# Optimization experiments

Measured on AMD Instinct MI355X. Metric: run time of the kernel, lower is better.

## Reference

```python
import jax, jax.numpy as jnp
import numpy as np

B, N, CIN, COUT, NS, S = 16, 512, 512, 512, 16, 8
EPS = 1e-5


def _bn(y, g, b):
    # eval-mode BatchNorm1d: running_mean=0, running_var=1 (fresh module buffers)
    return y * (g / jnp.sqrt(1.0 + EPS)) + b


def setup_inputs():
    key = jax.random.key(0)
    ks = jax.random.split(key, 16)

    def lin(k, fi, fo):
        kw, kb = jax.random.split(k)
        s = 1.0 / np.sqrt(fi)
        return (jax.random.uniform(kw, (fi, fo), minval=-s, maxval=s),
                jax.random.uniform(kb, (fo,), minval=-s, maxval=s))

    Wq, bq = lin(ks[0], CIN, COUT)
    Wk, bk = lin(ks[1], CIN, COUT)
    Wv, bv = lin(ks[2], CIN, COUT)
    p1_W, p1_b = lin(ks[3], 3, 3)
    p2_W, p2_b = lin(ks[4], 3, COUT)
    w1_W, w1_b = lin(ks[5], COUT, COUT // S)
    w2_W, w2_b = lin(ks[6], COUT // S, COUT // S)
    return dict(
        p=jax.random.uniform(ks[7], (B, N, 3)),
        x=jax.random.normal(ks[8], (B, CIN, N)),
        Wq=Wq, bq=bq, Wk=Wk, bk=bk, Wv=Wv, bv=bv,
        p1_W=p1_W, p1_b=p1_b,
        p_bn_g=1.0 + 0.1 * jax.random.normal(ks[9], (3,)),
        p_bn_b=0.1 * jax.random.normal(ks[10], (3,)),
        p2_W=p2_W, p2_b=p2_b,
        w_bn1_g=1.0 + 0.1 * jax.random.normal(ks[11], (COUT,)),
        w_bn1_b=0.1 * jax.random.normal(ks[12], (COUT,)),
        w1_W=w1_W, w1_b=w1_b,
        w_bn2_g=1.0 + 0.1 * jax.random.normal(ks[13], (COUT // S,)),
        w_bn2_b=0.1 * jax.random.normal(ks[14], (COUT // S,)),
        w2_W=w2_W, w2_b=w2_b,
    )


def reference(p, x, Wq, bq, Wk, bk, Wv, bv, p1_W, p1_b, p_bn_g, p_bn_b,
              p2_W, p2_b, w_bn1_g, w_bn1_b, w1_W, w1_b, w_bn2_g, w_bn2_b,
              w2_W, w2_b):
    xt = x.transpose(0, 2, 1)                     # (B,N,CIN)
    xq = xt @ Wq + bq                             # (B,N,COUT)
    xk = xt @ Wk + bk
    xv = xt @ Wv + bv
    # kNN over points (self-query): squared distances, then 16 smallest
    sq = jnp.sum(p * p, axis=-1)                  # (B,N)
    d = sq[:, :, None] + sq[:, None, :] - 2.0 * jnp.einsum('bnd,bmd->bnm', p, p)
    _, idx = jax.lax.top_k(-d, NS)                # (B,N,NS), includes self
    gather = jax.vmap(lambda f, i: f[i])          # per-batch fancy gather
    k_g = gather(xk, idx)                         # (B,N,NS,COUT)
    v_g = gather(xv, idx)                         # (B,N,NS,COUT)
    p_r = gather(p, idx) - p[:, :, None, :]       # relative coords (B,N,NS,3)
    # linear_p: Linear(3,3) -> BN(3) -> ReLU -> Linear(3,COUT)
    pr = jax.nn.relu(_bn(p_r @ p1_W + p1_b, p_bn_g, p_bn_b)) @ p2_W + p2_b
    # vector attention logits; out_planes//mid_planes == 1 so the .sum(3) is identity
    w = k_g - xq[:, :, None, :] + pr              # (B,N,NS,COUT)
    # linear_w: BN -> ReLU -> Linear(C, C//s) -> BN -> ReLU -> Linear(C//s, C//s)
    w = jax.nn.relu(_bn(w, w_bn1_g, w_bn1_b)) @ w1_W + w1_b
    w = jax.nn.relu(_bn(w, w_bn2_g, w_bn2_b)) @ w2_W + w2_b
    w = jax.nn.softmax(w, axis=2)                 # softmax over neighbors
    out = ((v_g + pr).reshape(B, N, NS, S, COUT // S)
           * w[:, :, :, None, :]).sum(2)          # (B,N,S,COUT//S)
    return out.reshape(B, N, COUT)
```

## Files before the change

kernel.cpp:

```cpp
#include <hip/hip_runtime.h>

typedef unsigned short u16;
typedef unsigned int   u32;

#define Bv  16
#define Nv  512
#define Cv  512
#define NSv 16
#define CCv 64

typedef __attribute__((ext_vector_type(8))) short bf16x8;
typedef __attribute__((ext_vector_type(4))) float f32x4;

__device__ __forceinline__ u16 f2bf(float f) {
  u32 b = __float_as_uint(f);
  return (u16)((b + 0x7fffu + ((b >> 16) & 1u)) >> 16);
}
__device__ __forceinline__ u32 pack2(float lo, float hi) {
  return (u32)f2bf(lo) | ((u32)f2bf(hi) << 16);
}
__device__ __forceinline__ u32 cvtpk(float lo, float hi) {
  u32 r;
  asm("v_cvt_pk_bf16_f32 %0, %1, %2" : "=v"(r) : "v"(lo), "v"(hi));
  return r;
}
__device__ __forceinline__ float bfl(u32 w) { return __uint_as_float(w << 16); }
__device__ __forceinline__ float bfh(u32 w) { return __uint_as_float(w & 0xffff0000u); }

#define GLD_LDS16(gp, lp)                                                              \
  __builtin_amdgcn_global_load_lds(                                                    \
      (const __attribute__((address_space(1))) u32*)(const void*)(gp),                 \
      (__attribute__((address_space(3))) u32*)(lp), 16, 0, 0)

__global__ __launch_bounds__(256) void prep_kernel(
    const float* __restrict__ p, int* __restrict__ idx_out,
    const float* __restrict__ x,
    const float* __restrict__ Wq, const float* __restrict__ Wk, const float* __restrict__ Wv,
    const float* __restrict__ w1W, const float* __restrict__ w2W,
    u16* __restrict__ xbT, u16* __restrict__ Wcat,
    u16* __restrict__ w1p, u16* __restrict__ w2p) {
  __shared__ __align__(16) char ARB[16640];
  const int t = threadIdx.x;
  if (blockIdx.x < 256) {
#pragma clang fp contract(off)
    float4* pnts = (float4*)ARB;
    const int b  = blockIdx.x >> 4;
    const int q0 = (blockIdx.x & 15) * 32;
    for (int e = t; e < Nv; e += 256) {
      float xx = p[(b * Nv + e) * 3 + 0];
      float yy = p[(b * Nv + e) * 3 + 1];
      float zz = p[(b * Nv + e) * 3 + 2];
      float s = ((xx * xx) + (yy * yy)) + (zz * zz);
      pnts[e] = make_float4(xx, yy, zz, s);
    }
    __syncthreads();
    const int q  = q0 + (t >> 3);
    const int pt = t & 7;
    const float4 qp = pnts[q];
    float bd[NSv]; int bi[NSv];
#pragma unroll
    for (int i = 0; i < NSv; i++) { bd[i] = 1e30f; bi[i] = 0; }
    const int m0 = pt * 64;
#pragma unroll 1
    for (int i = 0; i < 64; i++) {
      const int m = m0 + i;
      const float4 c = pnts[m];
      float dot = __builtin_fmaf(qp.z, c.z, __builtin_fmaf(qp.y, c.y, qp.x * c.x));
      float d = (qp.w + c.w) - (2.0f * dot);
      bool cm[NSv];
#pragma unroll
      for (int j = 0; j < NSv; j++) cm[j] = bd[j] > d;
#pragma unroll
      for (int j = NSv - 1; j > 0; j--) {
        bd[j] = cm[j - 1] ? bd[j - 1] : (cm[j] ? d : bd[j]);
        bi[j] = cm[j - 1] ? bi[j - 1] : (cm[j] ? m : bi[j]);
      }
      bd[0] = cm[0] ? d : bd[0];
      bi[0] = cm[0] ? m : bi[0];
    }
    int h = 0;
#pragma unroll 1
    for (int s = 0; s < 16; s++) {
      float mv = bd[0]; int ml = pt;
      {
        float ov = __shfl_xor(mv, 1); int ol = __shfl_xor(ml, 1);
        bool tk = (ov < mv) || (ov == mv && ol < ml);
        mv = tk ? ov : mv; ml = tk ? ol : ml;
      }
      {
        float ov = __shfl_xor(mv, 2); int ol = __shfl_xor(ml, 2);
        bool tk = (ov < mv) || (ov == mv && ol < ml);
        mv = tk ? ov : mv; ml = tk ? ol : ml;
      }
      {
        float ov = __shfl_xor(mv, 4); int ol = __shfl_xor(ml, 4);
        bool tk = (ov < mv) || (ov == mv && ol < ml);
        mv = tk ? ov : mv; ml = tk ? ol : ml;
      }
      if (ml == pt) {
#pragma unroll
        for (int j = 0; j < 15; j++) bd[j] = bd[j + 1];
        bd[15] = 1e30f;
        h++;
      }
    }
    const int lane = t & 63, gbase = lane & 56;
    int pre = 0;
#pragma unroll
    for (int j = 0; j < 7; j++) {
      int hj = __shfl(h, gbase + j);
      if (j < pt) pre += hj;
    }
    int* o = idx_out + (b * Nv + q) * NSv + pre;
#pragma unroll
    for (int j = 0; j < 16; j++)
      if (j < h) o[j] = bi[j];
  } else {
    float (*lt)[65] = (float(*)[65])ARB;
    const int id = blockIdx.x - 256;
    const int tile = id & 63, unit = id >> 6;
    const float* src; u16* dst;
    int k0, c0, srcC, dstC;
    if (unit < 16) {
      src = x + unit * 262144; dst = xbT + unit * 262144;
      k0 = (tile & 7) * 64; c0 = (tile >> 3) * 64; srcC = 512; dstC = 512;
    } else if (unit < 19) {
      const int mat = unit - 16;
      src = (mat == 0) ? Wq : (mat == 1) ? Wk : Wv;
      dst = Wcat + mat * 262144;
      k0 = (tile & 7) * 64; c0 = (tile >> 3) * 64; srcC = 512; dstC = 512;
    } else {
      if (tile < 8)       { src = w1W; dst = w1p; k0 = tile * 64; c0 = 0; srcC = 64; dstC = 512; }
      else if (tile == 8) { src = w2W; dst = w2p; k0 = 0; c0 = 0; srcC = 64; dstC = 64; }
      else return;
    }
    {
      const int r = t >> 2, cq = (t & 3) * 16;
      const float* s = src + (k0 + r) * srcC + c0 + cq;
#pragma unroll
      for (int i = 0; i < 4; i++) {
        const float4 v = *(const float4*)&s[i * 4];
        lt[r][cq + i * 4 + 0] = v.x;
        lt[r][cq + i * 4 + 1] = v.y;
        lt[r][cq + i * 4 + 2] = v.z;
        lt[r][cq + i * 4 + 3] = v.w;
      }
    }
    __syncthreads();
    {
      const int rr = t >> 2, kq = (t & 3) * 16;
      uint4 pa, pb;
      pa.x = pack2(lt[kq + 0][rr],  lt[kq + 1][rr]);
      pa.y = pack2(lt[kq + 2][rr],  lt[kq + 3][rr]);
      pa.z = pack2(lt[kq + 4][rr],  lt[kq + 5][rr]);
      pa.w = pack2(lt[kq + 6][rr],  lt[kq + 7][rr]);
      pb.x = pack2(lt[kq + 8][rr],  lt[kq + 9][rr]);
      pb.y = pack2(lt[kq + 10][rr], lt[kq + 11][rr]);
      pb.z = pack2(lt[kq + 12][rr], lt[kq + 13][rr]);
      pb.w = pack2(lt[kq + 14][rr], lt[kq + 15][rr]);
      u16* o = dst + (c0 + rr) * dstC + k0 + kq;
      *(uint4*)&o[0] = pa;
      *(uint4*)&o[8] = pb;
    }
  }
}

__global__ __launch_bounds__(256) void qkv_mfma(
    const u16* __restrict__ xbT, const u16* __restrict__ Wcat,
    const float* __restrict__ bq, const float* __restrict__ bk, const float* __restrict__ bv,
    const float* __restrict__ bn1g, const float* __restrict__ bn1b, const float* __restrict__ p2b,
    u16* __restrict__ xqh, u16* __restrict__ xkh, float* __restrict__ xv) {
  __shared__ u32 Sh[2][5120];
  const float rno = 1.0f / sqrtf(1.0f + 1e-5f);
  const int mt  = blockIdx.x;
  const int b   = mt >> 2;
  const int m0c = (mt & 3) * 128;
  const int j0  = blockIdx.y * 64;
  const int t   = threadIdx.x;
  const int lane = t & 63, w = t >> 6;
  const int l15 = lane & 15, quad = lane >> 4;

  const u16* asrc[2];
#pragma unroll
  for (int rd = 0; rd < 2; rd++) {
    const int gidx = rd * 256 + t;
    const int r = gidx >> 2, g = gidx & 3;
    const int gd = g ^ (r & 3) ^ ((r >> 2) & 3);
    asrc[rd] = xbT + (b * 512 + m0c + r) * 512 + gd * 8;
  }
  const u16* wsrc[3];
#pragma unroll
  for (int rd = 0; rd < 3; rd++) {
    const int gidx = rd * 256 + t;
    const int r = gidx >> 2, g = gidx & 3;
    const int gd = g ^ (r & 3) ^ ((r >> 2) & 3);
    wsrc[rd] = Wcat + (r >> 6) * 262144 + (j0 + (r & 63)) * 512 + gd * 8;
  }

  f32x4 acc[4][3][2];
#pragma unroll
  for (int a1 = 0; a1 < 4; a1++)
#pragma unroll
    for (int a2 = 0; a2 < 3; a2++)
#pragma unroll
      for (int a3 = 0; a3 < 2; a3++) acc[a1][a2][a3] = (f32x4){0.f, 0.f, 0.f, 0.f};

  const int sa  = (quad ^ (l15 & 3) ^ ((l15 >> 2) & 3)) * 4;
  const int ra0 = ((2 * w + 0) * 16 + l15) * 16;
  const int ra1 = ((2 * w + 1) * 16 + l15) * 16;

  auto stage = [&](int buf, int k0) {
#pragma unroll
    for (int rd = 0; rd < 2; rd++)
      GLD_LDS16(asrc[rd] + k0, &Sh[buf][(rd * 256 + w * 64) * 4]);
#pragma unroll
    for (int rd = 0; rd < 3; rd++)
      GLD_LDS16(wsrc[rd] + k0, &Sh[buf][2048 + (rd * 256 + w * 64) * 4]);
  };
  auto mfma_step = [&](int buf) {
    const u32* S = Sh[buf];
    const bf16x8 a0 = *(const bf16x8*)&S[ra0 + sa];
    const bf16x8 a1 = *(const bf16x8*)&S[ra1 + sa];
#pragma unroll
    for (int js = 0; js < 4; js++)
#pragma unroll
      for (int mat = 0; mat < 3; mat++) {
        const bf16x8 bfr = *(const bf16x8*)&S[2048 + (mat * 64 + js * 16 + l15) * 16 + sa];
        acc[js][mat][0] = __builtin_amdgcn_mfma_f32_16x16x32_bf16(a0, bfr, acc[js][mat][0], 0, 0, 0);
        acc[js][mat][1] = __builtin_amdgcn_mfma_f32_16x16x32_bf16(a1, bfr, acc[js][mat][1], 0, 0, 0);
      }
  };

  stage(0, 0);
  asm volatile("s_waitcnt vmcnt(0)" ::: "memory");
  __syncthreads();
  int cur = 0;
  for (int k0 = 0; k0 < 512; k0 += 32) {
    if (k0 + 32 < 512) stage(cur ^ 1, k0 + 32);
    mfma_step(cur);
    asm volatile("s_waitcnt vmcnt(0)" ::: "memory");
    __syncthreads();
    cur ^= 1;
  }

  float bias[4][3], s1v[4], Tv[4];
#pragma unroll
  for (int js = 0; js < 4; js++) {
    const int col = j0 + js * 16 + l15;
    bias[js][0] = bq[col];
    bias[js][1] = bk[col];
    bias[js][2] = bv[col];
    s1v[js] = bn1g[col] * rno;
    Tv[js]  = fmaf(p2b[col], s1v[js], bn1b[col]);
  }
#pragma unroll
  for (int js = 0; js < 4; js++)
#pragma unroll
    for (int mat = 0; mat < 3; mat++) {
      const int col = j0 + js * 16 + l15;
#pragma unroll
      for (int st = 0; st < 2; st++) {
        const int rbase = b * 512 + m0c + (2 * w + st) * 16 + quad * 4;
        const f32x4 v = acc[js][mat][st];
        if (mat == 2) {
#pragma unroll
          for (int reg = 0; reg < 4; reg++)
            xv[(rbase + reg) * 512 + col] = v[reg] + bias[js][2];
        } else if (mat == 0) {
#pragma unroll
          for (int reg = 0; reg < 4; reg++)
            xqh[(rbase + reg) * 512 + col] = f2bf((v[reg] + bias[js][0]) * s1v[js] - Tv[js]);
        } else {
#pragma unroll
          for (int reg = 0; reg < 4; reg++)
            xkh[(rbase + reg) * 512 + col] = f2bf((v[reg] + bias[js][1]) * s1v[js]);
        }
      }
    }
}

#define NQ  8
#define LSd 66

__global__ __launch_bounds__(256, 3) void attn_kernel(
    const float* __restrict__ p, const int* __restrict__ idx,
    const u16* __restrict__ xqh, const u16* __restrict__ xkh, const float* __restrict__ xv,
    const float* __restrict__ p1W, const float* __restrict__ p1b,
    const float* __restrict__ pbg, const float* __restrict__ pbb,
    const float* __restrict__ p2W, const float* __restrict__ p2b,
    const float* __restrict__ bn1g, const float* __restrict__ bn1b,
    const u16* __restrict__ w1p, const float* __restrict__ w1b,
    const float* __restrict__ bn2g, const float* __restrict__ bn2b,
    const u16* __restrict__ w2p, const float* __restrict__ w2b,
    float* __restrict__ out) {
  const float rno = 1.0f / sqrtf(1.0f + 1e-5f);
  const int s_  = blockIdx.x;
  const int xcd = s_ & 7, kk_ = s_ >> 3;
  const int b   = (xcd << 1) | (kk_ & 1);
  const int n0  = (kk_ >> 1) * NQ;
  const int t  = threadIdx.x;
  __shared__ float ARN[8448];
  __shared__ float h_s[128][3];
  __shared__ int   idx_s[128];
  float* A0f = ARN;
  float* A1f = ARN + 512;
  float* A2f = ARN + 1024;
  u32* wbf = (u32*)(ARN + 1536);
  u32* ubf = (u32*)(ARN + 3584);

  if (t < 128) idx_s[t] = idx[(b * Nv + n0 + (t >> 4)) * NSv + (t & 15)] & (Nv - 1);

  {
    const int c0 = t * 2;
#pragma unroll
    for (int i = 0; i < 2; i++) {
      const int c = c0 + i;
      const float s1 = bn1g[c] * rno;
      A0f[c] = p2W[c] * s1;
      A1f[c] = p2W[512 + c] * s1;
      A2f[c] = p2W[1024 + c] * s1;
    }
  }
  __syncthreads();

  for (int e = t; e < 384; e += 256) {
    const int row = e / 3, j = e % 3;
    const int m = idx_s[row];
    const int n = n0 + (row >> 4);
    float d0 = p[(b * Nv + m) * 3 + 0] - p[(b * Nv + n) * 3 + 0];
    float d1 = p[(b * Nv + m) * 3 + 1] - p[(b * Nv + n) * 3 + 1];
    float d2 = p[(b * Nv + m) * 3 + 2] - p[(b * Nv + n) * 3 + 2];
    float y = d0 * p1W[0 * 3 + j] + d1 * p1W[1 * 3 + j] + d2 * p1W[2 * 3 + j] + p1b[j];
    y = y * (pbg[j] * rno) + pbb[j];
    h_s[row][j] = fmaxf(y, 0.0f);
  }

  const int row = t >> 1, ci = (t & 1) * 32;
  const int mrow = idx_s[row];
  const u16* xkr = xkh + (b * Nv + mrow) * Cv + ci;
  const u16* xqr = xqh + (b * Nv + n0 + (row >> 4)) * Cv + ci;
  uint4 pf[4], pfq[4];
#pragma unroll
  for (int i = 0; i < 4; i++) {
    pf[i]  = *(const uint4*)&xkr[i * 8];
    pfq[i] = *(const uint4*)&xqr[i * 8];
  }
  __syncthreads();

  const int lane = t & 63, w = t >> 6;
  const int l15 = lane & 15, quad = lane >> 4;
  const float h0 = h_s[row][0], h1 = h_s[row][1], h2 = h_s[row][2];
  const int rsw = row & 7, half4 = (t & 1) * 4;

  int wrow[2], wg[2], wgd[2];
#pragma unroll
  for (int rd = 0; rd < 2; rd++) {
    const int gidx = rd * 256 + t;
    wrow[rd] = gidx >> 3; wg[rd] = gidx & 7; wgd[rd] = wg[rd] ^ (wrow[rd] & 7);
  }

  f32x4 acc[2][4];
#pragma unroll
  for (int a1 = 0; a1 < 2; a1++)
#pragma unroll
    for (int a2 = 0; a2 < 4; a2++) acc[a1][a2] = (f32x4){0.f, 0.f, 0.f, 0.f};

  for (int kc = 0; kc < Cv; kc += 64) {
    uint4 wr[2];
#pragma unroll
    for (int rd = 0; rd < 2; rd++)
      wr[rd] = *(const uint4*)&w1p[wrow[rd] * 512 + kc + wgd[rd] * 8];
    {
      u32* ub = &ubf[row * 32];
#pragma unroll
      for (int gi = 0; gi < 4; gi++) {
        const int c4 = kc + ci + gi * 8;
        const float4 A0a = *(const float4*)&A0f[c4], A0b = *(const float4*)&A0f[c4 + 4];
        const float4 A1a = *(const float4*)&A1f[c4], A1b = *(const float4*)&A1f[c4 + 4];
        const float4 A2a = *(const float4*)&A2f[c4], A2b = *(const float4*)&A2f[c4 + 4];
        const uint4 kw = pf[gi], qw = pfq[gi];
        const float d0 = bfl(kw.x) - bfl(qw.x);
        const float d1 = bfh(kw.x) - bfh(qw.x);
        const float d2 = bfl(kw.y) - bfl(qw.y);
        const float d3 = bfh(kw.y) - bfh(qw.y);
        const float d4 = bfl(kw.z) - bfl(qw.z);
        const float d5 = bfh(kw.z) - bfh(qw.z);
        const float d6 = bfl(kw.w) - bfl(qw.w);
        const float d7 = bfh(kw.w) - bfh(qw.w);
        const float u0 = fmaxf(fmaf(h0, A0a.x, fmaf(h1, A1a.x, fmaf(h2, A2a.x, d0))), 0.f);
        const float u1 = fmaxf(fmaf(h0, A0a.y, fmaf(h1, A1a.y, fmaf(h2, A2a.y, d1))), 0.f);
        const float u2 = fmaxf(fmaf(h0, A0a.z, fmaf(h1, A1a.z, fmaf(h2, A2a.z, d2))), 0.f);
        const float u3 = fmaxf(fmaf(h0, A0a.w, fmaf(h1, A1a.w, fmaf(h2, A2a.w, d3))), 0.f);
        const float u4 = fmaxf(fmaf(h0, A0b.x, fmaf(h1, A1b.x, fmaf(h2, A2b.x, d4))), 0.f);
        const float u5 = fmaxf(fmaf(h0, A0b.y, fmaf(h1, A1b.y, fmaf(h2, A2b.y, d5))), 0.f);
        const float u6 = fmaxf(fmaf(h0, A0b.z, fmaf(h1, A1b.z, fmaf(h2, A2b.z, d6))), 0.f);
        const float u7 = fmaxf(fmaf(h0, A0b.w, fmaf(h1, A1b.w, fmaf(h2, A2b.w, d7))), 0.f);
        uint4 pk;
        pk.x = cvtpk(u0, u1); pk.y = cvtpk(u2, u3);
        pk.z = cvtpk(u4, u5); pk.w = cvtpk(u6, u7);
        *(uint4*)&ub[((half4 + gi) ^ rsw) * 4] = pk;
      }
    }
    if (kc + 64 < Cv) {
#pragma unroll
      for (int i = 0; i < 4; i++) {
        pf[i]  = *(const uint4*)&xkr[kc + 64 + i * 8];
        pfq[i] = *(const uint4*)&xqr[kc + 64 + i * 8];
      }
    }
#pragma unroll
    for (int rd = 0; rd < 2; rd++)
      *(uint4*)&wbf[wrow[rd] * 32 + wg[rd] * 4] = wr[rd];
    __syncthreads();
#pragma unroll
    for (int ks = 0; ks < 2; ks++) {
      const int sw = ((ks * 4 + quad) ^ (l15 & 7)) * 4;
      const bf16x8 a0 = *(const bf16x8*)&ubf[((2 * w + 0) * 16 + l15) * 32 + sw];
      const bf16x8 a1 = *(const bf16x8*)&ubf[((2 * w + 1) * 16 + l15) * 32 + sw];
#pragma unroll
      for (int js = 0; js < 4; js++) {
        const bf16x8 bfr = *(const bf16x8*)&wbf[(js * 16 + l15) * 32 + sw];
        acc[0][js] = __builtin_amdgcn_mfma_f32_16x16x32_bf16(a0, bfr, acc[0][js], 0, 0, 0);
        acc[1][js] = __builtin_amdgcn_mfma_f32_16x16x32_bf16(a1, bfr, acc[1][js], 0, 0, 0);
      }
    }
    __syncthreads();
  }

  {
    u16* r1h = (u16*)ubf;
#pragma unroll
    for (int js = 0; js < 4; js++) {
      const int j = js * 16 + l15;
      const float wb = w1b[j], s2 = bn2g[j] * rno, b2 = bn2b[j];
      const int gph = j >> 3;
#pragma unroll
      for (int st = 0; st < 2; st++) {
        const int rbase = (2 * w + st) * 16 + quad * 4;
#pragma unroll
        for (int reg = 0; reg < 4; reg++) {
          const int r = rbase + reg;
          const float v = fmaxf((acc[st][js][reg] + wb) * s2 + b2, 0.f);
          r1h[r * 64 + (gph ^ (r & 7)) * 8 + (j & 7)] = f2bf(v);
        }
      }
    }
  }
#pragma unroll
  for (int rd = 0; rd < 2; rd++) {
    const uint4 v = *(const uint4*)&w2p[wrow[rd] * 64 + wgd[rd] * 8];
    *(uint4*)&wbf[wrow[rd] * 32 + wg[rd] * 4] = v;
  }
  __syncthreads();

  f32x4 acc2[2][4];
#pragma unroll
  for (int a1 = 0; a1 < 2; a1++)
#pragma unroll
    for (int a2 = 0; a2 < 4; a2++) acc2[a1][a2] = (f32x4){0.f, 0.f, 0.f, 0.f};
#pragma unroll
  for (int ks = 0; ks < 2; ks++) {
    const int sw = ((ks * 4 + quad) ^ (l15 & 7)) * 4;
    const bf16x8 a0 = *(const bf16x8*)&ubf[((2 * w + 0) * 16 + l15) * 32 + sw];
    const bf16x8 a1 = *(const bf16x8*)&ubf[((2 * w + 1) * 16 + l15) * 32 + sw];
#pragma unroll
    for (int js = 0; js < 4; js++) {
      const bf16x8 bfr = *(const bf16x8*)&wbf[(js * 16 + l15) * 32 + sw];
      acc2[0][js] = __builtin_amdgcn_mfma_f32_16x16x32_bf16(a0, bfr, acc2[0][js], 0, 0, 0);
      acc2[1][js] = __builtin_amdgcn_mfma_f32_16x16x32_bf16(a1, bfr, acc2[1][js], 0, 0, 0);
    }
  }
  __syncthreads();

  {
    float* lg = ARN;
#pragma unroll
    for (int js = 0; js < 4; js++) {
      const float wb2 = w2b[js * 16 + l15];
#pragma unroll
      for (int st = 0; st < 2; st++) {
        const int rbase = (2 * w + st) * 16 + quad * 4;
#pragma unroll
        for (int reg = 0; reg < 4; reg++)
          lg[(rbase + reg) * LSd + js * 16 + l15] = acc2[st][js][reg] + wb2;
      }
    }
  }
  __syncthreads();

#pragma unroll
  for (int pp = 0; pp < 2; pp++) {
    const int pair = t + pp * 256;
    const int q = pair >> 6, jj = pair & 63;
    float* base = &ARN[(q * 16) * LSd + jj];
    float v[NSv];
#pragma unroll
    for (int k = 0; k < NSv; k++) v[k] = base[k * LSd];
    float mx = v[0];
#pragma unroll
    for (int k = 1; k < NSv; k++) mx = fmaxf(mx, v[k]);
    float s = 0.0f;
#pragma unroll
    for (int k = 0; k < NSv; k++) { v[k] = expf(v[k] - mx); s += v[k]; }
    const float is = 1.0f / s;
#pragma unroll
    for (int k = 0; k < NSv; k++) base[k * LSd] = v[k] * is;
  }
  __syncthreads();

  {
    const int q = t >> 5, cb = t & 31;
    float hk0[NSv], hk1[NSv], hk2[NSv];
    int mk[NSv];
#pragma unroll
    for (int k = 0; k < NSv; k++) {
      hk0[k] = h_s[q * 16 + k][0];
      hk1[k] = h_s[q * 16 + k][1];
      hk2[k] = h_s[q * 16 + k][2];
      mk[k]  = idx_s[q * 16 + k];
    }
    const float* smb = &ARN[(q * 16) * LSd];
    float* ob = out + (b * Nv + n0 + q) * Cv;
#pragma unroll 1
    for (int i = 0; i < 16; i++) {
      const int c = cb + i * 32;
      const float pa = p2W[c], pb2 = p2W[512 + c], pc = p2W[1024 + c], pd = p2b[c];
      const int jj = c & 63;
      float s0 = 0.f, s1 = 0.f, s2 = 0.f, s3 = 0.f;
#pragma unroll
      for (int k = 0; k < NSv; k += 4) {
        const float pr0 = hk0[k + 0] * pa + hk1[k + 0] * pb2 + hk2[k + 0] * pc + pd;
        const float pr1 = hk0[k + 1] * pa + hk1[k + 1] * pb2 + hk2[k + 1] * pc + pd;
        const float pr2 = hk0[k + 2] * pa + hk1[k + 2] * pb2 + hk2[k + 2] * pc + pd;
        const float pr3 = hk0[k + 3] * pa + hk1[k + 3] * pb2 + hk2[k + 3] * pc + pd;
        s0 = fmaf(xv[(b * Nv + mk[k + 0]) * Cv + c] + pr0, smb[(k + 0) * LSd + jj], s0);
        s1 = fmaf(xv[(b * Nv + mk[k + 1]) * Cv + c] + pr1, smb[(k + 1) * LSd + jj], s1);
        s2 = fmaf(xv[(b * Nv + mk[k + 2]) * Cv + c] + pr2, smb[(k + 2) * LSd + jj], s2);
        s3 = fmaf(xv[(b * Nv + mk[k + 3]) * Cv + c] + pr3, smb[(k + 3) * LSd + jj], s3);
      }
      ob[c] = (s0 + s1) + (s2 + s3);
    }
  }
}

extern "C" void kernel_launch(void* const* d_in, const int* in_sizes, int n_in,
                              void* d_out, int out_size, void* d_ws, size_t ws_size,
                              hipStream_t stream) {
  const float* p    = (const float*)d_in[0];
  const float* x    = (const float*)d_in[1];
  const float* Wq   = (const float*)d_in[2];
  const float* bq   = (const float*)d_in[3];
  const float* Wk   = (const float*)d_in[4];
  const float* bk   = (const float*)d_in[5];
  const float* Wv   = (const float*)d_in[6];
  const float* bv   = (const float*)d_in[7];
  const float* p1W  = (const float*)d_in[8];
  const float* p1b  = (const float*)d_in[9];
  const float* pbg  = (const float*)d_in[10];
  const float* pbb  = (const float*)d_in[11];
  const float* p2W  = (const float*)d_in[12];
  const float* p2b  = (const float*)d_in[13];
  const float* bn1g = (const float*)d_in[14];
  const float* bn1b = (const float*)d_in[15];
  const float* w1W  = (const float*)d_in[16];
  const float* w1b  = (const float*)d_in[17];
  const float* bn2g = (const float*)d_in[18];
  const float* bn2b = (const float*)d_in[19];
  const float* w2W  = (const float*)d_in[20];
  const float* w2b  = (const float*)d_in[21];

  int*   idxb = (int*)d_ws;
  float* xv   = (float*)((char*)d_ws + 524288);
  u16*   xqh  = (u16*)(xv + 8192 * 512);
  u16*   xkh  = xqh + 8192 * 512;
  u16*   xbT  = xkh + 8192 * 512;
  u16*   Wcat = xbT + 8192 * 512;
  u16*   w1p  = Wcat + 3 * 512 * 512;
  u16*   w2p  = w1p + 64 * 512;

  prep_kernel<<<dim3(1536), 256, 0, stream>>>(p, idxb, x, Wq, Wk, Wv, w1W, w2W,
                                              xbT, Wcat, w1p, w2p);
  qkv_mfma<<<dim3(64, 8), 256, 0, stream>>>(xbT, Wcat, bq, bk, bv, bn1g, bn1b, p2b,
                                            xqh, xkh, xv);
  attn_kernel<<<dim3(1024), 256, 0, stream>>>(p, idxb, xqh, xkh, xv,
                                              p1W, p1b, pbg, pbb, p2W, p2b,
                                              bn1g, bn1b, w1p, w1b, bn2g, bn2b,
                                              w2p, w2b, (float*)d_out);
}
```

Before: 231.9 us.

## Halve attention block query tile and factor positional term out of aggregation

Halves the queries per attention block from eight to four, doubling the grid and raising the occupancy target to five blocks per CU with smaller shared-memory buffers. Each wave now does one MFMA row tile instead of two. The final aggregation uses the fact that softmax weights sum over neighbors. It precomputes softmax-weighted sums of the hidden position features once and applies p2W to them per channel, instead of rebuilding the positional encoding for each neighbor and channel. Softmax also switches to fast __expf. The cost is more redundant per-block weight loading and w1 staging.

Result: faster. 216.4 us (median of 3 runs) (-6.7%).

```diff
diff --git a/kernel.cpp b/kernel.cpp
--- a/kernel.cpp
+++ b/kernel.cpp
@@ -279,10 +279,10 @@
     }
 }
 
-#define NQ  8
+#define NQ  4
 #define LSd 66
 
-__global__ __launch_bounds__(256, 3) void attn_kernel(
+__global__ __launch_bounds__(256, 5) void attn_kernel(
     const float* __restrict__ p, const int* __restrict__ idx,
     const u16* __restrict__ xqh, const u16* __restrict__ xkh, const float* __restrict__ xv,
     const float* __restrict__ p1W, const float* __restrict__ p1b,
@@ -299,16 +299,16 @@
   const int b   = (xcd << 1) | (kk_ & 1);
   const int n0  = (kk_ >> 1) * NQ;
   const int t  = threadIdx.x;
-  __shared__ float ARN[8448];
-  __shared__ float h_s[128][3];
-  __shared__ int   idx_s[128];
+  __shared__ float ARN[5632];
+  __shared__ float h_s[64][3];
+  __shared__ int   idx_s[64];
   float* A0f = ARN;
   float* A1f = ARN + 512;
   float* A2f = ARN + 1024;
   u32* wbf = (u32*)(ARN + 1536);
   u32* ubf = (u32*)(ARN + 3584);
 
-  if (t < 128) idx_s[t] = idx[(b * Nv + n0 + (t >> 4)) * NSv + (t & 15)] & (Nv - 1);
+  if (t < 64) idx_s[t] = idx[(b * Nv + n0 + (t >> 4)) * NSv + (t & 15)] & (Nv - 1);
 
   {
     const int c0 = t * 2;
@@ -323,8 +323,8 @@
   }
   __syncthreads();
 
-  for (int e = t; e < 384; e += 256) {
-    const int row = e / 3, j = e % 3;
+  if (t < 192) {
+    const int row = t / 3, j = t % 3;
     const int m = idx_s[row];
     const int n = n0 + (row >> 4);
     float d0 = p[(b * Nv + m) * 3 + 0] - p[(b * Nv + n) * 3 + 0];
@@ -335,13 +335,13 @@
     h_s[row][j] = fmaxf(y, 0.0f);
   }
 
-  const int row = t >> 1, ci = (t & 1) * 32;
+  const int row = t >> 2, ci = (t & 3) * 16;
   const int mrow = idx_s[row];
   const u16* xkr = xkh + (b * Nv + mrow) * Cv + ci;
   const u16* xqr = xqh + (b * Nv + n0 + (row >> 4)) * Cv + ci;
-  uint4 pf[4], pfq[4];
-#pragma unroll
-  for (int i = 0; i < 4; i++) {
+  uint4 pf[2], pfq[2];
+#pragma unroll
+  for (int i = 0; i < 2; i++) {
     pf[i]  = *(const uint4*)&xkr[i * 8];
     pfq[i] = *(const uint4*)&xqr[i * 8];
   }
@@ -350,7 +350,7 @@
   const int lane = t & 63, w = t >> 6;
   const int l15 = lane & 15, quad = lane >> 4;
   const float h0 = h_s[row][0], h1 = h_s[row][1], h2 = h_s[row][2];
-  const int rsw = row & 7, half4 = (t & 1) * 4;
+  const int rsw = row & 7, g0 = (t & 3) * 2;
 
   int wrow[2], wg[2], wgd[2];
 #pragma unroll
@@ -359,11 +359,9 @@
     wrow[rd] = gidx >> 3; wg[rd] = gidx & 7; wgd[rd] = wg[rd] ^ (wrow[rd] & 7);
   }
 
-  f32x4 acc[2][4];
-#pragma unroll
-  for (int a1 = 0; a1 < 2; a1++)
-#pragma unroll
-    for (int a2 = 0; a2 < 4; a2++) acc[a1][a2] = (f32x4){0.f, 0.f, 0.f, 0.f};
+  f32x4 acc[4];
+#pragma unroll
+  for (int a2 = 0; a2 < 4; a2++) acc[a2] = (f32x4){0.f, 0.f, 0.f, 0.f};
 
   for (int kc = 0; kc < Cv; kc += 64) {
     uint4 wr[2];
@@ -373,7 +371,7 @@
     {
       u32* ub = &ubf[row * 32];
 #pragma unroll
-      for (int gi = 0; gi < 4; gi++) {
+      for (int gi = 0; gi < 2; gi++) {
         const int c4 = kc + ci + gi * 8;
         const float4 A0a = *(const float4*)&A0f[c4], A0b = *(const float4*)&A0f[c4 + 4];
         const float4 A1a = *(const float4*)&A1f[c4], A1b = *(const float4*)&A1f[c4 + 4];
@@ -398,12 +396,12 @@
         uint4 pk;
         pk.x = cvtpk(u0, u1); pk.y = cvtpk(u2, u3);
         pk.z = cvtpk(u4, u5); pk.w = cvtpk(u6, u7);
-        *(uint4*)&ub[((half4 + gi) ^ rsw) * 4] = pk;
+        *(uint4*)&ub[((g0 + gi) ^ rsw) * 4] = pk;
       }
     }
     if (kc + 64 < Cv) {
 #pragma unroll
-      for (int i = 0; i < 4; i++) {
+      for (int i = 0; i < 2; i++) {
         pf[i]  = *(const uint4*)&xkr[kc + 64 + i * 8];
         pfq[i] = *(const uint4*)&xqr[kc + 64 + i * 8];
       }
@@ -415,13 +413,11 @@
 #pragma unroll
     for (int ks = 0; ks < 2; ks++) {
       const int sw = ((ks * 4 + quad) ^ (l15 & 7)) * 4;
-      const bf16x8 a0 = *(const bf16x8*)&ubf[((2 * w + 0) * 16 + l15) * 32 + sw];
-      const bf16x8 a1 = *(const bf16x8*)&ubf[((2 * w + 1) * 16 + l15) * 32 + sw];
+      const bf16x8 a0 = *(const bf16x8*)&ubf[(w * 16 + l15) * 32 + sw];
 #pragma unroll
       for (int js = 0; js < 4; js++) {
         const bf16x8 bfr = *(const bf16x8*)&wbf[(js * 16 + l15) * 32 + sw];
-        acc[0][js] = __builtin_amdgcn_mfma_f32_16x16x32_bf16(a0, bfr, acc[0][js], 0, 0, 0);
-        acc[1][js] = __builtin_amdgcn_mfma_f32_16x16x32_bf16(a1, bfr, acc[1][js], 0, 0, 0);
+        acc[js] = __builtin_amdgcn_mfma_f32_16x16x32_bf16(a0, bfr, acc[js], 0, 0, 0);
       }
     }
     __syncthreads();
@@ -434,15 +430,12 @@
       const int j = js * 16 + l15;
       const float wb = w1b[j], s2 = bn2g[j] * rno, b2 = bn2b[j];
       const int gph = j >> 3;
-#pragma unroll
-      for (int st = 0; st < 2; st++) {
-        const int rbase = (2 * w + st) * 16 + quad * 4;
-#pragma unroll
-        for (int reg = 0; reg < 4; reg++) {
-          const int r = rbase + reg;
-          const float v = fmaxf((acc[st][js][reg] + wb) * s2 + b2, 0.f);
-          r1h[r * 64 + (gph ^ (r & 7)) * 8 + (j & 7)] = f2bf(v);
-        }
+      const int rbase = w * 16 + quad * 4;
+#pragma unroll
+      for (int reg = 0; reg < 4; reg++) {
+        const int r = rbase + reg;
+        const float v = fmaxf((acc[js][reg] + wb) * s2 + b2, 0.f);
+        r1h[r * 64 + (gph ^ (r & 7)) * 8 + (j & 7)] = f2bf(v);
       }
     }
   }
@@ -453,21 +446,17 @@
   }
   __syncthreads();
 
-  f32x4 acc2[2][4];
-#pragma unroll
-  for (int a1 = 0; a1 < 2; a1++)
-#pragma unroll
-    for (int a2 = 0; a2 < 4; a2++) acc2[a1][a2] = (f32x4){0.f, 0.f, 0.f, 0.f};
+  f32x4 acc2[4];
+#pragma unroll
+  for (int a2 = 0; a2 < 4; a2++) acc2[a2] = (f32x4){0.f, 0.f, 0.f, 0.f};
 #pragma unroll
   for (int ks = 0; ks < 2; ks++) {
     const int sw = ((ks * 4 + quad) ^ (l15 & 7)) * 4;
-    const bf16x8 a0 = *(const bf16x8*)&ubf[((2 * w + 0) * 16 + l15) * 32 + sw];
-    const bf16x8 a1 = *(const bf16x8*)&ubf[((2 * w + 1) * 16 + l15) * 32 + sw];
+    const bf16x8 a0 = *(const bf16x8*)&ubf[(w * 16 + l15) * 32 + sw];
 #pragma unroll
     for (int js = 0; js < 4; js++) {
       const bf16x8 bfr = *(const bf16x8*)&wbf[(js * 16 + l15) * 32 + sw];
-      acc2[0][js] = __builtin_amdgcn_mfma_f32_16x16x32_bf16(a0, bfr, acc2[0][js], 0, 0, 0);
-      acc2[1][js] = __builtin_amdgcn_mfma_f32_16x16x32_bf16(a1, bfr, acc2[1][js], 0, 0, 0);
+      acc2[js] = __builtin_amdgcn_mfma_f32_16x16x32_bf16(a0, bfr, acc2[js], 0, 0, 0);
     }
   }
   __syncthreads();
@@ -477,21 +466,16 @@
 #pragma unroll
     for (int js = 0; js < 4; js++) {
       const float wb2 = w2b[js * 16 + l15];
-#pragma unroll
-      for (int st = 0; st < 2; st++) {
-        const int rbase = (2 * w + st) * 16 + quad * 4;
-#pragma unroll
-        for (int reg = 0; reg < 4; reg++)
-          lg[(rbase + reg) * LSd + js * 16 + l15] = acc2[st][js][reg] + wb2;
-      }
-    }
-  }
-  __syncthreads();
-
-#pragma unroll
-  for (int pp = 0; pp < 2; pp++) {
-    const int pair = t + pp * 256;
-    const int q = pair >> 6, jj = pair & 63;
+      const int rbase = w * 16 + quad * 4;
+#pragma unroll
+      for (int reg = 0; reg < 4; reg++)
+        lg[(rbase + reg) * LSd + js * 16 + l15] = acc2[js][reg] + wb2;
+    }
+  }
+  __syncthreads();
+
+  {
+    const int q = t >> 6, jj = t & 63;
     float* base = &ARN[(q * 16) * LSd + jj];
     float v[NSv];
 #pragma unroll
@@ -501,7 +485,7 @@
     for (int k = 1; k < NSv; k++) mx = fmaxf(mx, v[k]);
     float s = 0.0f;
 #pragma unroll
-    for (int k = 0; k < NSv; k++) { v[k] = expf(v[k] - mx); s += v[k]; }
+    for (int k = 0; k < NSv; k++) { v[k] = __expf(v[k] - mx); s += v[k]; }
     const float is = 1.0f / s;
 #pragma unroll
     for (int k = 0; k < NSv; k++) base[k * LSd] = v[k] * is;
@@ -509,36 +493,38 @@
   __syncthreads();
 
   {
-    const int q = t >> 5, cb = t & 31;
-    float hk0[NSv], hk1[NSv], hk2[NSv];
+    const int q = t >> 6, cb = t & 63;
     int mk[NSv];
+    float smv[NSv];
+    float H0 = 0.f, H1 = 0.f, H2 = 0.f;
+    const float* smb = &ARN[(q * 16) * LSd];
 #pragma unroll
     for (int k = 0; k < NSv; k++) {
-      hk0[k] = h_s[q * 16 + k][0];
-      hk1[k] = h_s[q * 16 + k][1];
-      hk2[k] = h_s[q * 16 + k][2];
-      mk[k]  = idx_s[q * 16 + k];
-    }
-    const float* smb = &ARN[(q * 16) * LSd];
+      mk[k] = idx_s[q * 16 + k];
+      const float s0 = smb[k * LSd + cb];
+      smv[k] = s0;
+      H0 = fmaf(h_s[q * 16 + k][0], s0, H0);
+      H1 = fmaf(h_s[q * 16 + k][1], s0, H1);
+      H2 = fmaf(h_s[q * 16 + k][2], s0, H2);
+    }
     float* ob = out + (b * Nv + n0 + q) * Cv;
+    const float* xvb = xv + b * Nv * Cv;
 #pragma unroll 1
-    for (int i = 0; i < 16; i++) {
-      const int c = cb + i * 32;
-      const float pa = p2W[c], pb2 = p2W[512 + c], pc = p2W[1024 + c], pd = p2b[c];
-      const int jj = c & 63;
+    for (int ii = 0; ii < 8; ii++) {
+      const int c = cb + ii * 64;
       float s0 = 0.f, s1 = 0.f, s2 = 0.f, s3 = 0.f;
 #pragma unroll
       for (int k = 0; k < NSv; k += 4) {
-        const float pr0 = hk0[k + 0] * pa + hk1[k + 0] * pb2 + hk2[k + 0] * pc + pd;
-        const float pr1 = hk0[k + 1] * pa + hk1[k + 1] * pb2 + hk2[k + 1] * pc + pd;
-        const float pr2 = hk0[k + 2] * pa + hk1[k + 2] * pb2 + hk2[k + 2] * pc + pd;
-        const float pr3 = hk0[k + 3] * pa + hk1[k + 3] * pb2 + hk2[k + 3] * pc + pd;
-        s0 = fmaf(xv[(b * Nv + mk[k + 0]) * Cv + c] + pr0, smb[(k + 0) * LSd + jj], s0);
-        s1 = fmaf(xv[(b * Nv + mk[k + 1]) * Cv + c] + pr1, smb[(k + 1) * LSd + jj], s1);
-        s2 = fmaf(xv[(b * Nv + mk[k + 2]) * Cv + c] + pr2, smb[(k + 2) * LSd + jj], s2);
-        s3 = fmaf(xv[(b * Nv + mk[k + 3]) * Cv + c] + pr3, smb[(k + 3) * LSd + jj], s3);
-      }
-      ob[c] = (s0 + s1) + (s2 + s3);
+        s0 = fmaf(xvb[mk[k + 0] * Cv + c], smv[k + 0], s0);
+        s1 = fmaf(xvb[mk[k + 1] * Cv + c], smv[k + 1], s1);
+        s2 = fmaf(xvb[mk[k + 2] * Cv + c], smv[k + 2], s2);
+        s3 = fmaf(xvb[mk[k + 3] * Cv + c], smv[k + 3], s3);
+      }
+      float r = (s0 + s1) + (s2 + s3);
+      r = fmaf(p2W[c], H0, r);
+      r = fmaf(p2W[512 + c], H1, r);
+      r = fmaf(p2W[1024 + c], H2, r);
+      ob[c] = r + p2b[c];
     }
   }
 }
@@ -582,7 +568,7 @@
                                               xbT, Wcat, w1p, w2p);
   qkv_mfma<<<dim3(64, 8), 256, 0, stream>>>(xbT, Wcat, bq, bk, bv, bn1g, bn1b, p2b,
                                             xqh, xkh, xv);
-  attn_kernel<<<dim3(1024), 256, 0, stream>>>(p, idxb, xqh, xkh, xv,
+  attn_kernel<<<dim3(2048), 256, 0, stream>>>(p, idxb, xqh, xkh, xv,
                                               p1W, p1b, pbg, pbb, p2W, p2b,
                                               bn1g, bn1b, w1p, w1b, bn2g, bn2b,
                                               w2p, w2b, (float*)d_out);
```
